# Optimization experiments

Measured on AMD Instinct MI355X. Metric: run time of the kernel, lower is better.

## Reference

```python
import jax, jax.numpy as jnp
import numpy as np

B, C, H, W = 16, 256, 64, 64
DA = 64  # attention_size


def setup_inputs() -> dict:
    key = jax.random.key(0)
    ks = jax.random.split(key, 7)
    s_in = 1.0 / np.sqrt(C)
    return {
        "x": jax.random.normal(ks[0], (B, C, H, W), jnp.float32),
        "Wq": jax.random.normal(ks[1], (DA, C), jnp.float32) * s_in,
        "bq": jax.random.normal(ks[2], (DA,), jnp.float32) * 0.01,
        "Wk": jax.random.normal(ks[3], (DA, C), jnp.float32) * s_in,
        "bk": jax.random.normal(ks[4], (DA,), jnp.float32) * 0.01,
        "Wv": jax.random.normal(ks[5], (C, C), jnp.float32) * s_in,
        "bv": jax.random.normal(ks[6], (C,), jnp.float32) * 0.01,
    }


def reference(x, Wq, bq, Wk, bk, Wv, bv):
    b, c, h, w = x.shape
    n = h * w
    xf = x.reshape(b, c, n)                      # [B,C,N]
    q = jnp.einsum('ac,bcn->ban', Wq, xf) + bq[None, :, None]   # [B,DA,N]
    k = jnp.einsum('ac,bcn->ban', Wk, xf) + bk[None, :, None]   # [B,DA,N]
    v = jnp.einsum('dc,bcn->bdn', Wv, xf) + bv[None, :, None]   # [B,C,N]
    # scores[b,i,j] = q[:,i] . k[:,j], scaled by 1/sqrt(H*W) (as in source)
    scores = jnp.einsum('bai,baj->bij', q, k) / jnp.sqrt(jnp.float32(n))
    attn = jax.nn.softmax(scores, axis=-1)       # [B,N,N]
    out = jnp.einsum('bcj,bij->bci', v, attn)    # [B,C,N]
    return out.reshape(b, c, h, w) + x
```

## Files before the change

kernel.cpp:

```cpp
#include <hip/hip_runtime.h>
#include <hip/hip_bf16.h>
#include <stdint.h>


#define B_  16
#define C_  256
#define N_  4096
#define DA_ 64
#define MSHIFT 2.0f

typedef __attribute__((ext_vector_type(8))) short short8;
typedef __attribute__((ext_vector_type(4))) float f32x4;

__device__ int g_isf32;

__device__ __forceinline__ short f2bf(float f) {
    union { float f; uint32_t u; } v; v.f = f;
    uint32_t r = v.u + 0x7fffu + ((v.u >> 16) & 1u);
    return (short)(r >> 16);
}
__device__ __forceinline__ float bf2f(uint16_t s) {
    union { uint32_t u; float f; } v; v.u = ((uint32_t)s) << 16;
    return v.f;
}
__device__ __forceinline__ uint32_t pkbf(float a, float b) {
    union { __hip_bfloat162 h; uint32_t u; } c;
    c.h = __float22bfloat162_rn(make_float2(a, b));
    return c.u;
}

__global__ void detect_kernel(const void* __restrict__ x) {
    const uint16_t* p = (const uint16_t*)x;
    int i = threadIdx.x;
    uint16_t u = p[2 * i];
    int e = (u >> 7) & 0xFF;
    unsigned long long m = __ballot(e >= 112 && e <= 132);
    if (i == 0) g_isf32 = (__popcll(m) < 32) ? 1 : 0;
}

template<bool F32>
__device__ __forceinline__ void proj_body(
    const void* __restrict__ xv,
    const void* __restrict__ Wqv, const void* __restrict__ bqv,
    const void* __restrict__ Wkv, const void* __restrict__ bkv,
    const void* __restrict__ Wvv, const void* __restrict__ bvv,
    uint16_t* __restrict__ Q, uint16_t* __restrict__ K, uint16_t* __restrict__ Vt,
    float* bias_lds, uint16_t* buf)
{
    const int tid = threadIdx.x;
    const int b  = blockIdx.x >> 6;
    const int n0 = (blockIdx.x & 63) * 64;
    const int w = tid >> 6, lane = tid & 63, q = lane >> 4, ln = lane & 15;

    for (int idx = tid; idx < 384; idx += 256) {
        float bias;
        if (F32) {
            bias = (idx < 64)  ? ((const float*)bqv)[idx]
                 : (idx < 128) ? ((const float*)bkv)[idx - 64]
                               : ((const float*)bvv)[idx - 128];
        } else {
            bias = (idx < 64)  ? bf2f(((const uint16_t*)bqv)[idx])
                 : (idx < 128) ? bf2f(((const uint16_t*)bkv)[idx - 64])
                               : bf2f(((const uint16_t*)bvv)[idx - 128]);
        }
        bias_lds[idx] = bias;
    }

    {
        int cbase = tid >> 2, s0 = tid & 3;
        #pragma unroll
        for (int cc = 0; cc < 4; cc++) {
            int c = cc * 64 + cbase;
            if (F32) {
                const float* xr = (const float*)xv + ((size_t)b * C_ + c) * N_ + n0;
                #pragma unroll
                for (int k = 0; k < 4; k++) {
                    int nl = (s0 + 4 * k) * 4;
                    float4 v = *(const float4*)(xr + nl);
                    buf[(nl + 0) * 264 + c] = (uint16_t)f2bf(v.x);
                    buf[(nl + 1) * 264 + c] = (uint16_t)f2bf(v.y);
                    buf[(nl + 2) * 264 + c] = (uint16_t)f2bf(v.z);
                    buf[(nl + 3) * 264 + c] = (uint16_t)f2bf(v.w);
                }
            } else {
                const uint16_t* xr = (const uint16_t*)xv + ((size_t)b * C_ + c) * N_ + n0;
                #pragma unroll
                for (int k = 0; k < 2; k++) {
                    int nl = s0 * 16 + k * 8;
                    short8 v = *(const short8*)(xr + nl);
                    #pragma unroll
                    for (int e = 0; e < 8; e++)
                        buf[(nl + e) * 264 + c] = (uint16_t)v[e];
                }
            }
        }
    }
    __syncthreads();

    f32x4 acc[6][4];
    #pragma unroll
    for (int mt = 0; mt < 6; mt++)
        #pragma unroll
        for (int nt = 0; nt < 4; nt++) acc[mt][nt] = (f32x4)0.0f;

    for (int kc = 0; kc < 8; kc++) {
        short8 af[6];
        #pragma unroll
        for (int mt = 0; mt < 6; mt++) {
            int row = (w * 6 + mt) * 16 + ln;
            if (F32) {
                const float* src = (row < 64) ? (const float*)Wqv + (size_t)row * 256
                                 : (row < 128) ? (const float*)Wkv + (size_t)(row - 64) * 256
                                               : (const float*)Wvv + (size_t)(row - 128) * 256;
                float4 a0 = *(const float4*)(src + kc * 32 + q * 8);
                float4 a1 = *(const float4*)(src + kc * 32 + q * 8 + 4);
                union { short8 s; uint32_t u[4]; } c;
                c.u[0] = pkbf(a0.x, a0.y); c.u[1] = pkbf(a0.z, a0.w);
                c.u[2] = pkbf(a1.x, a1.y); c.u[3] = pkbf(a1.z, a1.w);
                af[mt] = c.s;
            } else {
                const uint16_t* src = (row < 64) ? (const uint16_t*)Wqv + (size_t)row * 256
                                    : (row < 128) ? (const uint16_t*)Wkv + (size_t)(row - 64) * 256
                                                  : (const uint16_t*)Wvv + (size_t)(row - 128) * 256;
                af[mt] = *(const short8*)(src + kc * 32 + q * 8);
            }
        }
        short8 bfr[4];
        #pragma unroll
        for (int nt = 0; nt < 4; nt++)
            bfr[nt] = *(const short8*)&buf[(nt * 16 + ln) * 264 + kc * 32 + q * 8];
        #pragma unroll
        for (int mt = 0; mt < 6; mt++)
            #pragma unroll
            for (int nt = 0; nt < 4; nt++)
                acc[mt][nt] = __builtin_amdgcn_mfma_f32_16x16x32_bf16(
                    af[mt], bfr[nt], acc[mt][nt], 0, 0, 0);
    }
    __syncthreads();

    #pragma unroll
    for (int mt = 0; mt < 6; mt++) {
        int rowb = (w * 6 + mt) * 16 + q * 4;
        #pragma unroll
        for (int r = 0; r < 4; r++) {
            float bias = bias_lds[rowb + r];
            #pragma unroll
            for (int nt = 0; nt < 4; nt++)
                buf[(rowb + r) * 72 + nt * 16 + ln] =
                    (uint16_t)f2bf(acc[mt][nt][r] + bias);
        }
    }
    __syncthreads();

    {
        int a = tid & 63, nb = tid >> 6;
        uint16_t* Qb = Q + ((size_t)b * N_ + n0) * 64;
        uint16_t* Kb = K + ((size_t)b * N_ + n0) * 64;
        #pragma unroll 4
        for (int j = 0; j < 16; j++) {
            int n = nb + 4 * j;
            Qb[(size_t)n * 64 + a] = buf[a * 72 + n];
            Kb[(size_t)n * 64 + a] = buf[(64 + a) * 72 + n];
        }
    }
    {
        int ch = tid & 7;
        #pragma unroll
        for (int p = 0; p < 8; p++) {
            int c = p * 32 + (tid >> 3);
            short8 v = *(const short8*)&buf[(128 + c) * 72 + ch * 8];
            *(short8*)(Vt + ((size_t)b * C_ + c) * N_ + n0 + ch * 8) = v;
        }
    }
}

__global__ __launch_bounds__(256, 2) void proj_kernel(
    const void* xv, const void* Wqv, const void* bqv, const void* Wkv,
    const void* bkv, const void* Wvv, const void* bvv,
    uint16_t* Q, uint16_t* K, uint16_t* Vt)
{
    __shared__ float    bias_lds[384];
    __shared__ uint16_t buf[384 * 72];
    if (g_isf32) proj_body<true >(xv, Wqv, bqv, Wkv, bkv, Wvv, bvv, Q, K, Vt, bias_lds, buf);
    else         proj_body<false>(xv, Wqv, bqv, Wkv, bkv, Wvv, bvv, Q, K, Vt, bias_lds, buf);
}

template<bool F32>
__device__ __forceinline__ void flash_body(
    const uint16_t* __restrict__ Q, const uint16_t* __restrict__ K,
    const uint16_t* __restrict__ Vt, const void* __restrict__ xv,
    void* __restrict__ outv,
    uint16_t* Klds, uint16_t* Plds, float* l_lds)
{
    const int tid = threadIdx.x;
    const int b  = blockIdx.x >> 5;
    const int i0 = (blockIdx.x & 31) * 128;
    const int w = tid >> 6, lane = tid & 63, q = lane >> 4, ln = lane & 15;
    const int rw = w >> 2, cw = w & 3;

    const float c1 = 1.4426950408889634f / 64.0f;

    short8 qf[2];
    {
        const uint16_t* qrow = Q + ((size_t)b * N_ + (i0 + w * 16 + ln)) * 64;
        qf[0] = *(const short8*)(qrow + q * 8);
        qf[1] = *(const short8*)(qrow + 32 + q * 8);
    }

    const uint16_t* Kb = K + (size_t)b * N_ * 64;
    const uint16_t* vrow[4];
    #pragma unroll
    for (int ct = 0; ct < 4; ct++)
        vrow[ct] = Vt + ((size_t)b * C_ + (cw * 64 + ct * 16 + ln)) * N_ + q * 8;

    float l_run = 0.0f;
    f32x4 O[4][4];
    #pragma unroll
    for (int rg = 0; rg < 4; rg++)
        #pragma unroll
        for (int ct = 0; ct < 4; ct++) O[rg][ct] = (f32x4)0.0f;

    for (int it = 0; it < 64; it++) {
        const int j0 = it * 64;
        {
            int row = tid >> 3, ch = tid & 7;
            *(short8*)&Klds[row * 72 + ch * 8] =
                *(const short8*)(Kb + (size_t)(j0 + row) * 64 + ch * 8);
        }
        __syncthreads();

        f32x4 s[4];
        #pragma unroll
        for (int jt = 0; jt < 4; jt++) s[jt] = (f32x4)0.0f;
        #pragma unroll
        for (int kst = 0; kst < 2; kst++)
            #pragma unroll
            for (int jt = 0; jt < 4; jt++) {
                short8 kf = *(const short8*)&Klds[(jt * 16 + ln) * 72 + kst * 32 + q * 8];
                s[jt] = __builtin_amdgcn_mfma_f32_16x16x32_bf16(kf, qf[kst], s[jt], 0, 0, 0);
            }

        uint16_t* prow = &Plds[(w * 16 + ln) * 72 + q * 4];
        #pragma unroll
        for (int jt = 0; jt < 4; jt++) {
            float p0 = exp2f(s[jt][0] * c1 - MSHIFT);
            float p1 = exp2f(s[jt][1] * c1 - MSHIFT);
            float p2 = exp2f(s[jt][2] * c1 - MSHIFT);
            float p3 = exp2f(s[jt][3] * c1 - MSHIFT);
            l_run += (p0 + p1) + (p2 + p3);
            uint2 pk; pk.x = pkbf(p0, p1); pk.y = pkbf(p2, p3);
            *(uint2*)&prow[jt * 16] = pk;
        }
        __syncthreads();

        #pragma unroll
        for (int kst = 0; kst < 2; kst++) {
            short8 bfr[4];
            #pragma unroll
            for (int ct = 0; ct < 4; ct++)
                bfr[ct] = *(const short8*)(vrow[ct] + j0 + kst * 32);
            short8 af[4];
            #pragma unroll
            for (int rg = 0; rg < 4; rg++)
                af[rg] = *(const short8*)&Plds[(rw * 64 + rg * 16 + ln) * 72 + kst * 32 + q * 8];
            #pragma unroll
            for (int rg = 0; rg < 4; rg++)
                #pragma unroll
                for (int ct = 0; ct < 4; ct++)
                    O[rg][ct] = __builtin_amdgcn_mfma_f32_16x16x32_bf16(
                        af[rg], bfr[ct], O[rg][ct], 0, 0, 0);
        }
        __syncthreads();
    }

    l_run += __shfl_xor(l_run, 16);
    l_run += __shfl_xor(l_run, 32);
    if (lane < 16) l_lds[w * 16 + lane] = l_run;
    __syncthreads();

    #pragma unroll
    for (int rg = 0; rg < 4; rg++) {
        f32x4 lv = *(const f32x4*)&l_lds[rw * 64 + rg * 16 + q * 4];
        f32x4 li; li[0] = 1.0f/lv[0]; li[1] = 1.0f/lv[1]; li[2] = 1.0f/lv[2]; li[3] = 1.0f/lv[3];
        #pragma unroll
        for (int ct = 0; ct < 4; ct++) {
            int c = cw * 64 + ct * 16 + ln;
            size_t off = (size_t)c * N_ + i0 + rw * 64 + rg * 16 + q * 4;
            if (F32) {
                const float* xb = (const float*)xv + (size_t)b * C_ * N_;
                float* ob = (float*)outv + (size_t)b * C_ * N_;
                float4 xv4 = *(const float4*)(xb + off);
                float4 res;
                res.x = O[rg][ct][0] * li[0] + xv4.x;
                res.y = O[rg][ct][1] * li[1] + xv4.y;
                res.z = O[rg][ct][2] * li[2] + xv4.z;
                res.w = O[rg][ct][3] * li[3] + xv4.w;
                *(float4*)(ob + off) = res;
            } else {
                const uint16_t* xb = (const uint16_t*)xv + (size_t)b * C_ * N_;
                uint16_t* ob = (uint16_t*)outv + (size_t)b * C_ * N_;
                uint2 xp = *(const uint2*)(xb + off);
                uint2 res;
                res.x = pkbf(O[rg][ct][0] * li[0] + bf2f((uint16_t)(xp.x & 0xFFFF)),
                             O[rg][ct][1] * li[1] + bf2f((uint16_t)(xp.x >> 16)));
                res.y = pkbf(O[rg][ct][2] * li[2] + bf2f((uint16_t)(xp.y & 0xFFFF)),
                             O[rg][ct][3] * li[3] + bf2f((uint16_t)(xp.y >> 16)));
                *(uint2*)(ob + off) = res;
            }
        }
    }
}

__global__ __launch_bounds__(512, 4) void flash_kernel(
    const uint16_t* Q, const uint16_t* K, const uint16_t* Vt,
    const void* xv, void* outv)
{
    __shared__ uint16_t Klds[64 * 72];
    __shared__ uint16_t Plds[128 * 72];
    __shared__ __align__(16) float l_lds[128];
    if (g_isf32) flash_body<true >(Q, K, Vt, xv, outv, Klds, Plds, l_lds);
    else         flash_body<false>(Q, K, Vt, xv, outv, Klds, Plds, l_lds);
}

extern "C" void kernel_launch(void* const* d_in, const int* in_sizes, int n_in,
                              void* d_out, int out_size, void* d_ws, size_t ws_size,
                              hipStream_t stream) {
    const void* x  = d_in[0];
    const void* Wq = d_in[1];
    const void* bq = d_in[2];
    const void* Wk = d_in[3];
    const void* bk = d_in[4];
    const void* Wv = d_in[5];
    const void* bv = d_in[6];

    uint16_t* Qw = (uint16_t*)d_ws;
    uint16_t* Kw = Qw + (size_t)B_ * N_ * DA_;
    uint16_t* Vw = Kw + (size_t)B_ * N_ * DA_;

    detect_kernel<<<dim3(1), dim3(64), 0, stream>>>(x);
    proj_kernel<<<dim3(B_ * 64), dim3(256), 0, stream>>>(x, Wq, bq, Wk, bk, Wv, bv, Qw, Kw, Vw);
    flash_kernel<<<dim3(B_ * 32), dim3(512), 0, stream>>>(Qw, Kw, Vw, x, d_out);
}
```

Baseline: 491.1 us.

## Double-buffer K tiles via direct global-to-LDS loads with XOR swizzle

```diff
diff --git a/kernel.cpp b/kernel.cpp
--- a/kernel.cpp
+++ b/kernel.cpp
@@ -27,6 +27,13 @@
     union { __hip_bfloat162 h; uint32_t u; } c;
     c.h = __float22bfloat162_rn(make_float2(a, b));
     return c.u;
+}
+
+__device__ __forceinline__ void gld_lds16(const uint16_t* g, uint16_t* l) {
+    __builtin_amdgcn_global_load_lds(
+        (const __attribute__((address_space(1))) unsigned int*)g,
+        (__attribute__((address_space(3))) unsigned int*)l,
+        16, 0, 0);
 }
 
 __global__ void detect_kernel(const void* __restrict__ x) {
@@ -190,7 +197,7 @@
     const uint16_t* __restrict__ Q, const uint16_t* __restrict__ K,
     const uint16_t* __restrict__ Vt, const void* __restrict__ xv,
     void* __restrict__ outv,
-    uint16_t* Klds, uint16_t* Plds, float* l_lds)
+    uint16_t* Klds2, uint16_t* Plds, float* l_lds)
 {
     const int tid = threadIdx.x;
     const int b  = blockIdx.x >> 5;
@@ -213,6 +220,13 @@
     for (int ct = 0; ct < 4; ct++)
         vrow[ct] = Vt + ((size_t)b * C_ + (cw * 64 + ct * 16 + ln)) * N_ + q * 8;
 
+    const int krow = lane >> 3, kslot = lane & 7;
+    const size_t kgoff = (size_t)(w * 8 + krow) * 64 + (size_t)((kslot ^ krow) * 8);
+    uint16_t* kdst0 = Klds2 + (w << 9);
+
+    const int kb0 = ln * 64 + ((q ^ (ln & 7)) * 8);
+    const int kb1 = ln * 64 + (((4 + q) ^ (ln & 7)) * 8);
+
     float l_run = 0.0f;
     f32x4 O[4][4];
     #pragma unroll
@@ -220,25 +234,32 @@
         #pragma unroll
         for (int ct = 0; ct < 4; ct++) O[rg][ct] = (f32x4)0.0f;
 
+    gld_lds16(Kb + kgoff, kdst0);
+    __syncthreads();
+
     for (int it = 0; it < 64; it++) {
         const int j0 = it * 64;
-        {
-            int row = tid >> 3, ch = tid & 7;
-            *(short8*)&Klds[row * 72 + ch * 8] =
-                *(const short8*)(Kb + (size_t)(j0 + row) * 64 + ch * 8);
-        }
-        __syncthreads();
+        const int par = it & 1;
+
+        if (it < 63)
+            gld_lds16(Kb + (size_t)(j0 + 64) * 64 + kgoff,
+                      Klds2 + ((par ^ 1) << 12) + (w << 9));
+
+        const uint16_t* Kt = Klds2 + (par << 12);
 
         f32x4 s[4];
         #pragma unroll
         for (int jt = 0; jt < 4; jt++) s[jt] = (f32x4)0.0f;
-        #pragma unroll
-        for (int kst = 0; kst < 2; kst++)
-            #pragma unroll
-            for (int jt = 0; jt < 4; jt++) {
-                short8 kf = *(const short8*)&Klds[(jt * 16 + ln) * 72 + kst * 32 + q * 8];
-                s[jt] = __builtin_amdgcn_mfma_f32_16x16x32_bf16(kf, qf[kst], s[jt], 0, 0, 0);
-            }
+
+        __builtin_amdgcn_s_setprio(1);
+        #pragma unroll
+        for (int jt = 0; jt < 4; jt++) {
+            short8 kf0 = *(const short8*)(Kt + jt * 1024 + kb0);
+            s[jt] = __builtin_amdgcn_mfma_f32_16x16x32_bf16(kf0, qf[0], s[jt], 0, 0, 0);
+            short8 kf1 = *(const short8*)(Kt + jt * 1024 + kb1);
+            s[jt] = __builtin_amdgcn_mfma_f32_16x16x32_bf16(kf1, qf[1], s[jt], 0, 0, 0);
+        }
+        __builtin_amdgcn_s_setprio(0);
 
         uint16_t* prow = &Plds[(w * 16 + ln) * 72 + q * 4];
         #pragma unroll
@@ -253,6 +274,7 @@
         }
         __syncthreads();
 
+        __builtin_amdgcn_s_setprio(1);
         #pragma unroll
         for (int kst = 0; kst < 2; kst++) {
             short8 bfr[4];
@@ -270,6 +292,9 @@
                     O[rg][ct] = __builtin_amdgcn_mfma_f32_16x16x32_bf16(
                         af[rg], bfr[ct], O[rg][ct], 0, 0, 0);
         }
+        __builtin_amdgcn_s_setprio(0);
+
+        asm volatile("s_waitcnt vmcnt(0)" ::: "memory");
         __syncthreads();
     }
 
@@ -315,11 +340,11 @@
     const uint16_t* Q, const uint16_t* K, const uint16_t* Vt,
     const void* xv, void* outv)
 {
-    __shared__ uint16_t Klds[64 * 72];
+    __shared__ uint16_t Klds2[2 * 64 * 64];
     __shared__ uint16_t Plds[128 * 72];
     __shared__ __align__(16) float l_lds[128];
-    if (g_isf32) flash_body<true >(Q, K, Vt, xv, outv, Klds, Plds, l_lds);
-    else         flash_body<false>(Q, K, Vt, xv, outv, Klds, Plds, l_lds);
+    if (g_isf32) flash_body<true >(Q, K, Vt, xv, outv, Klds2, Plds, l_lds);
+    else         flash_body<false>(Q, K, Vt, xv, outv, Klds2, Plds, l_lds);
 }
 
 extern "C" void kernel_launch(void* const* d_in, const int* in_sizes, int n_in,
```

Result: slower. 522.4 us (+6.4%).

## Double-buffer K and P tiles, prefetch V early, remap blocks across XCDs

Applied to the files above, without the earlier changes.

```diff
diff --git a/kernel.cpp b/kernel.cpp
--- a/kernel.cpp
+++ b/kernel.cpp
@@ -190,11 +190,13 @@
     const uint16_t* __restrict__ Q, const uint16_t* __restrict__ K,
     const uint16_t* __restrict__ Vt, const void* __restrict__ xv,
     void* __restrict__ outv,
-    uint16_t* Klds, uint16_t* Plds, float* l_lds)
+    uint16_t* Klds2, uint16_t* Plds2, float* l_lds)
 {
     const int tid = threadIdx.x;
-    const int b  = blockIdx.x >> 5;
-    const int i0 = (blockIdx.x & 31) * 128;
+    const int d  = blockIdx.x;
+    const int xc = d & 7, kk = d >> 3;
+    const int b  = xc + ((kk >= 32) ? 8 : 0);
+    const int i0 = (kk & 31) * 128;
     const int w = tid >> 6, lane = tid & 63, q = lane >> 4, ln = lane & 15;
     const int rw = w >> 2, cw = w & 3;
 
@@ -208,10 +210,12 @@
     }
 
     const uint16_t* Kb = K + (size_t)b * N_ * 64;
-    const uint16_t* vrow[4];
-    #pragma unroll
-    for (int ct = 0; ct < 4; ct++)
-        vrow[ct] = Vt + ((size_t)b * C_ + (cw * 64 + ct * 16 + ln)) * N_ + q * 8;
+    const uint16_t* vr0 = Vt + ((size_t)b * C_ + (cw * 64 +  0 + ln)) * N_ + q * 8;
+    const uint16_t* vr1 = Vt + ((size_t)b * C_ + (cw * 64 + 16 + ln)) * N_ + q * 8;
+    const uint16_t* vr2 = Vt + ((size_t)b * C_ + (cw * 64 + 32 + ln)) * N_ + q * 8;
+    const uint16_t* vr3 = Vt + ((size_t)b * C_ + (cw * 64 + 48 + ln)) * N_ + q * 8;
+
+    const int krow = tid >> 3, kch = (tid & 7) * 8;
 
     float l_run = 0.0f;
     f32x4 O[4][4];
@@ -220,27 +224,44 @@
         #pragma unroll
         for (int ct = 0; ct < 4; ct++) O[rg][ct] = (f32x4)0.0f;
 
+    {
+        short8 k0 = *(const short8*)(Kb + (size_t)krow * 64 + kch);
+        *(short8*)&Klds2[krow * 72 + kch] = k0;
+    }
+    __syncthreads();
+
     for (int it = 0; it < 64; it++) {
         const int j0 = it * 64;
-        {
-            int row = tid >> 3, ch = tid & 7;
-            *(short8*)&Klds[row * 72 + ch * 8] =
-                *(const short8*)(Kb + (size_t)(j0 + row) * 64 + ch * 8);
-        }
-        __syncthreads();
+        const int cur = it & 1;
+        const uint16_t* Kc = Klds2 + cur * (64 * 72);
+        uint16_t*       Kn = Klds2 + (cur ^ 1) * (64 * 72);
+        uint16_t*       Pl = Plds2 + cur * (128 * 72);
+
+        short8 v00 = *(const short8*)(vr0 + j0);
+        short8 v01 = *(const short8*)(vr1 + j0);
+        short8 v02 = *(const short8*)(vr2 + j0);
+        short8 v03 = *(const short8*)(vr3 + j0);
+        short8 v10 = *(const short8*)(vr0 + j0 + 32);
+        short8 v11 = *(const short8*)(vr1 + j0 + 32);
+        short8 v12 = *(const short8*)(vr2 + j0 + 32);
+        short8 v13 = *(const short8*)(vr3 + j0 + 32);
+
+        short8 kreg;
+        if (it < 63)
+            kreg = *(const short8*)(Kb + (size_t)(j0 + 64 + krow) * 64 + kch);
 
         f32x4 s[4];
         #pragma unroll
         for (int jt = 0; jt < 4; jt++) s[jt] = (f32x4)0.0f;
         #pragma unroll
-        for (int kst = 0; kst < 2; kst++)
-            #pragma unroll
-            for (int jt = 0; jt < 4; jt++) {
-                short8 kf = *(const short8*)&Klds[(jt * 16 + ln) * 72 + kst * 32 + q * 8];
-                s[jt] = __builtin_amdgcn_mfma_f32_16x16x32_bf16(kf, qf[kst], s[jt], 0, 0, 0);
-            }
-
-        uint16_t* prow = &Plds[(w * 16 + ln) * 72 + q * 4];
+        for (int jt = 0; jt < 4; jt++) {
+            short8 kf0 = *(const short8*)&Kc[(jt * 16 + ln) * 72 + q * 8];
+            s[jt] = __builtin_amdgcn_mfma_f32_16x16x32_bf16(kf0, qf[0], s[jt], 0, 0, 0);
+            short8 kf1 = *(const short8*)&Kc[(jt * 16 + ln) * 72 + 32 + q * 8];
+            s[jt] = __builtin_amdgcn_mfma_f32_16x16x32_bf16(kf1, qf[1], s[jt], 0, 0, 0);
+        }
+
+        uint16_t* prow = &Pl[(w * 16 + ln) * 72 + q * 4];
         #pragma unroll
         for (int jt = 0; jt < 4; jt++) {
             float p0 = exp2f(s[jt][0] * c1 - MSHIFT);
@@ -251,26 +272,38 @@
             uint2 pk; pk.x = pkbf(p0, p1); pk.y = pkbf(p2, p3);
             *(uint2*)&prow[jt * 16] = pk;
         }
-        __syncthreads();
-
-        #pragma unroll
-        for (int kst = 0; kst < 2; kst++) {
-            short8 bfr[4];
-            #pragma unroll
-            for (int ct = 0; ct < 4; ct++)
-                bfr[ct] = *(const short8*)(vrow[ct] + j0 + kst * 32);
+
+        asm volatile("s_waitcnt lgkmcnt(0)\n\ts_barrier" ::: "memory");
+
+        {
             short8 af[4];
             #pragma unroll
             for (int rg = 0; rg < 4; rg++)
-                af[rg] = *(const short8*)&Plds[(rw * 64 + rg * 16 + ln) * 72 + kst * 32 + q * 8];
+                af[rg] = *(const short8*)&Pl[(rw * 64 + rg * 16 + ln) * 72 + q * 8];
+            #pragma unroll
+            for (int rg = 0; rg < 4; rg++) {
+                O[rg][0] = __builtin_amdgcn_mfma_f32_16x16x32_bf16(af[rg], v00, O[rg][0], 0, 0, 0);
+                O[rg][1] = __builtin_amdgcn_mfma_f32_16x16x32_bf16(af[rg], v01, O[rg][1], 0, 0, 0);
+                O[rg][2] = __builtin_amdgcn_mfma_f32_16x16x32_bf16(af[rg], v02, O[rg][2], 0, 0, 0);
+                O[rg][3] = __builtin_amdgcn_mfma_f32_16x16x32_bf16(af[rg], v03, O[rg][3], 0, 0, 0);
+            }
             #pragma unroll
             for (int rg = 0; rg < 4; rg++)
-                #pragma unroll
-                for (int ct = 0; ct < 4; ct++)
-                    O[rg][ct] = __builtin_amdgcn_mfma_f32_16x16x32_bf16(
-                        af[rg], bfr[ct], O[rg][ct], 0, 0, 0);
-        }
-        __syncthreads();
+                af[rg] = *(const short8*)&Pl[(rw * 64 + rg * 16 + ln) * 72 + 32 + q * 8];
+            #pragma unroll
+            for (int rg = 0; rg < 4; rg++) {
+                O[rg][0] = __builtin_amdgcn_mfma_f32_16x16x32_bf16(af[rg], v10, O[rg][0], 0, 0, 0);
+                O[rg][1] = __builtin_amdgcn_mfma_f32_16x16x32_bf16(af[rg], v11, O[rg][1], 0, 0, 0);
+                O[rg][2] = __builtin_amdgcn_mfma_f32_16x16x32_bf16(af[rg], v12, O[rg][2], 0, 0, 0);
+                O[rg][3] = __builtin_amdgcn_mfma_f32_16x16x32_bf16(af[rg], v13, O[rg][3], 0, 0, 0);
+            }
+        }
+
+        if (it < 63) {
+            asm volatile("s_waitcnt vmcnt(0)" ::: "memory");
+            *(short8*)&Kn[krow * 72 + kch] = kreg;
+        }
+        asm volatile("s_waitcnt lgkmcnt(0)\n\ts_barrier" ::: "memory");
     }
 
     l_run += __shfl_xor(l_run, 16);
@@ -311,15 +344,15 @@
     }
 }
 
-__global__ __launch_bounds__(512, 4) void flash_kernel(
+__global__ __launch_bounds__(512, 2) void flash_kernel(
     const uint16_t* Q, const uint16_t* K, const uint16_t* Vt,
     const void* xv, void* outv)
 {
-    __shared__ uint16_t Klds[64 * 72];
-    __shared__ uint16_t Plds[128 * 72];
+    __shared__ uint16_t Klds2[2 * 64 * 72];
+    __shared__ uint16_t Plds2[2 * 128 * 72];
     __shared__ __align__(16) float l_lds[128];
-    if (g_isf32) flash_body<true >(Q, K, Vt, xv, outv, Klds, Plds, l_lds);
-    else         flash_body<false>(Q, K, Vt, xv, outv, Klds, Plds, l_lds);
+    if (g_isf32) flash_body<true >(Q, K, Vt, xv, outv, Klds2, Plds2, l_lds);
+    else         flash_body<false>(Q, K, Vt, xv, outv, Klds2, Plds2, l_lds);
 }
 
 extern "C" void kernel_launch(void* const* d_in, const int* in_sizes, int n_in,
```

New measurement: 482.4 us. About the same (-1.8%).
